# Kernel optimization log

Hardware: AMD Instinct MI355X
Metric: run time of the kernel (lower is better)

## Reference

```python
import jax, jax.numpy as jnp
import numpy as np
from jax import lax

ALPHA = 0.2  # LeakyReLU negative slope


def setup_inputs() -> dict:
    key = jax.random.key(0)
    k1, k2, k3, k4, k5 = jax.random.split(key, 5)
    B, Cin, N, L = 16, 64, 1024, 12
    Cout, Kt = 64, 3
    inp = jax.random.normal(k1, (B, Cin, N, L), dtype=jnp.float32)
    adj = jax.random.normal(k2, (B, N, N), dtype=jnp.float32)
    w0 = jax.random.normal(k3, (Cout, Cin, 1, Kt), dtype=jnp.float32) * (1.0 / np.sqrt(Cin * Kt))
    b0 = jax.random.normal(k4, (Cout,), dtype=jnp.float32) * 0.01
    w1 = jax.random.normal(k5, (1, Cout * L, 1), dtype=jnp.float32) * (1.0 / np.sqrt(Cout * L))
    return {"input": inp, "adj": adj, "w0": w0, "b0": b0, "w1": w1}


def reference(input, adj, w0, b0, w1):
    # conv0: Conv2d(in,out,(1,Kt),padding=(0,1)) -> (B, Cout, N, L)
    x = lax.conv_general_dilated(
        input, w0, window_strides=(1, 1), padding=((0, 0), (1, 1)),
        dimension_numbers=("NCHW", "OIHW", "NCHW"))
    x = x + b0[None, :, None, None]
    B, C, N, L = x.shape
    # permute(0,1,3,2).view(B, C*L, N): channel-major over (C, L)
    x1 = jnp.transpose(x, (0, 1, 3, 2)).reshape(B, C * L, N)
    # conv1 (k=1, no bias) applied twice (original uses conv1 for both f_1 and f_2)
    f = jnp.einsum('bkn,k->bn', x1, w1[0, :, 0])  # (B, N)
    # logits[b,i,j] = f_1[b,0,j] + f_2[b,i,0]
    logits = f[:, None, :] + f[:, :, None]  # (B, N, N)
    z = jnp.where(logits >= 0, logits, ALPHA * logits) + adj
    attention = jax.nn.softmax(z, axis=-1)
    attention = jnp.swapaxes(attention, -1, -2)  # (B, N, N)
    h_prime = jnp.einsum('bcnl,bnq->bcql', x, attention)
    return h_prime, attention
```

## Files before the change

kernel.cpp:

```cpp
#include <hip/hip_runtime.h>
#include <stdint.h>

typedef unsigned short ushort_t;
typedef unsigned int uint_t;

#define B_SZ 16
#define CIN 64
#define COUT 64
#define N_SZ 1024
#define L_SZ 12
#define CL 768
#define ALPHA 0.2f

typedef __bf16 bf16x8 __attribute__((ext_vector_type(8)));
typedef float floatx4 __attribute__((ext_vector_type(4)));

__device__ __forceinline__ ushort_t f2bf(float x) {
    uint_t u = __float_as_uint(x);
    u += 0x7fffu + ((u >> 16) & 1u);
    return (ushort_t)(u >> 16);
}
__device__ __forceinline__ float bf2f(ushort_t h) {
    return __uint_as_float(((uint_t)h) << 16);
}

__global__ __launch_bounds__(256) void conv_f_kernel(
    const float* __restrict__ inp, const float* __restrict__ w0,
    const float* __restrict__ b0, const float* __restrict__ w1,
    ushort_t* __restrict__ Xt, float* __restrict__ fout)
{
    __shared__ float Din[4 * 64 * 15];
    __shared__ float w0L[64 * 16 * 3];
    __shared__ float w1L[16 * 12];
    __shared__ float fred[256];

    const int n0 = blockIdx.x * 64;
    const int cb = blockIdx.y * 16;
    const int b  = blockIdx.z;
    const int t  = threadIdx.x;
    const int n_l = t & 63, ct = t >> 6;

    for (int idx = t; idx < 3072; idx += 256) {
        const int co_l = idx / 192, rem = idx - co_l * 192;
        const int ci = rem / 3, kt = rem - ci * 3;
        w0L[ci * 48 + co_l * 3 + kt] = w0[cb * 192 + idx];
    }
    if (t < 192) w1L[t] = w1[cb * 12 + t];
    for (int q = t; q < 512; q += 256) {
        const int ci = q >> 7, r = q & 127;
        Din[ci * 960 + (r & 63) * 15 + ((r >> 6) ? 13 : 0)] = 0.f;
    }

    float acc[4][12];
#pragma unroll
    for (int c = 0; c < 4; c++)
#pragma unroll
        for (int l = 0; l < 12; l++) acc[c][l] = 0.f;

    const float* inpB = inp + (size_t)b * CIN * N_SZ * L_SZ + n0 * 12;

    for (int cc = 0; cc < 16; cc++) {
        __syncthreads();
#pragma unroll
        for (int it = 0; it < 3; it++) {
            const int idx = it * 256 + t;
            const int ci_c = idx / 192, r = idx - ci_c * 192;
            const int n = r / 3, lg = r - n * 3;
            const float4 v = *(const float4*)(
                inpB + (size_t)(cc * 4 + ci_c) * (N_SZ * L_SZ) + n * 12 + lg * 4);
            float* d = &Din[ci_c * 960 + n * 15 + 1 + lg * 4];
            d[0] = v.x; d[1] = v.y; d[2] = v.z; d[3] = v.w;
        }
        __syncthreads();
#pragma unroll
        for (int cl = 0; cl < 4; cl++) {
            const int ci = cc * 4 + cl;
            const float* row = &Din[cl * 960 + n_l * 15];
            float p[14];
#pragma unroll
            for (int s = 0; s < 14; s++) p[s] = row[s];
            const float* wr = &w0L[ci * 48 + ct * 12];
#pragma unroll
            for (int c = 0; c < 4; c++) {
                const float wa = wr[c * 3], wb = wr[c * 3 + 1], wc = wr[c * 3 + 2];
#pragma unroll
                for (int l = 0; l < 12; l++)
                    acc[c][l] = fmaf(p[l], wa,
                                fmaf(p[l + 1], wb,
                                fmaf(p[l + 2], wc, acc[c][l])));
            }
        }
    }

    const int n = n0 + n_l;
    ushort_t* XtB = Xt + (size_t)b * CL * N_SZ + n;
    float fp = 0.f;
#pragma unroll
    for (int c = 0; c < 4; c++) {
        const int co_l = ct * 4 + c;
        const float b0v = b0[cb + co_l];
#pragma unroll
        for (int l = 0; l < 12; l++) {
            const float x = acc[c][l] + b0v;
            fp += x * w1L[co_l * 12 + l];
            XtB[(size_t)((cb + co_l) * 12 + l) * N_SZ] = f2bf(x);
        }
    }
    fred[t] = fp;
    __syncthreads();
    if (t < 64) {
        const float s = fred[t] + fred[t + 64] + fred[t + 128] + fred[t + 192];
        atomicAdd(&fout[b * N_SZ + n0 + t], s);
    }
}

__global__ __launch_bounds__(256) void softmax_kernel(
    const float* __restrict__ adj, const float* __restrict__ f,
    ushort_t* __restrict__ Sb)
{
    __shared__ float smx[4], sms[4];
    const int i = blockIdx.x, b = blockIdx.y, t = threadIdx.x;
    const int lane = t & 63, wv = t >> 6;

    const float* frow = f + b * N_SZ;
    const float fi = frow[i];
    const float4 fj = *(const float4*)(frow + 4 * t);
    const float4 av = *(const float4*)(adj + ((size_t)b * N_SZ + i) * N_SZ + 4 * t);

    float z[4];
    z[0] = fi + fj.x; z[1] = fi + fj.y; z[2] = fi + fj.z; z[3] = fi + fj.w;
#pragma unroll
    for (int k = 0; k < 4; k++) z[k] = (z[k] >= 0.f) ? z[k] : ALPHA * z[k];
    z[0] += av.x; z[1] += av.y; z[2] += av.z; z[3] += av.w;

    float mx = fmaxf(fmaxf(z[0], z[1]), fmaxf(z[2], z[3]));
#pragma unroll
    for (int o = 32; o; o >>= 1) mx = fmaxf(mx, __shfl_xor(mx, o, 64));
    if (lane == 0) smx[wv] = mx;
    __syncthreads();
    mx = fmaxf(fmaxf(smx[0], smx[1]), fmaxf(smx[2], smx[3]));

    float e[4], s = 0.f;
#pragma unroll
    for (int k = 0; k < 4; k++) { e[k] = __expf(z[k] - mx); s += e[k]; }
#pragma unroll
    for (int o = 32; o; o >>= 1) s += __shfl_xor(s, o, 64);
    if (lane == 0) sms[wv] = s;
    __syncthreads();
    s = sms[0] + sms[1] + sms[2] + sms[3];
    const float inv = 1.0f / s;

    const uint_t p0 = (uint_t)f2bf(e[0] * inv) | ((uint_t)f2bf(e[1] * inv) << 16);
    const uint_t p1 = (uint_t)f2bf(e[2] * inv) | ((uint_t)f2bf(e[3] * inv) << 16);
    uint2 pk; pk.x = p0; pk.y = p1;
    *(uint2*)&Sb[((size_t)b * N_SZ + i) * N_SZ + 4 * t] = pk;
}

__global__ __launch_bounds__(256) void att_transpose_kernel(
    const ushort_t* __restrict__ Sb, float* __restrict__ att)
{
    __shared__ float T[64][65];
    const int b = blockIdx.z;
    const int i0 = blockIdx.x * 64, j0 = blockIdx.y * 64;
    const int t = threadIdx.x;

#pragma unroll
    for (int ph = 0; ph < 2; ph++) {
        const int idx = ph * 256 + t;
        const int r = idx >> 3, c8 = (idx & 7) * 8;
        const uint4 v = *(const uint4*)(Sb + ((size_t)b * N_SZ + i0 + r) * N_SZ + j0 + c8);
        T[r][c8 + 0] = bf2f((ushort_t)(v.x & 0xffff));
        T[r][c8 + 1] = bf2f((ushort_t)(v.x >> 16));
        T[r][c8 + 2] = bf2f((ushort_t)(v.y & 0xffff));
        T[r][c8 + 3] = bf2f((ushort_t)(v.y >> 16));
        T[r][c8 + 4] = bf2f((ushort_t)(v.z & 0xffff));
        T[r][c8 + 5] = bf2f((ushort_t)(v.z >> 16));
        T[r][c8 + 6] = bf2f((ushort_t)(v.w & 0xffff));
        T[r][c8 + 7] = bf2f((ushort_t)(v.w >> 16));
    }
    __syncthreads();
#pragma unroll
    for (int ph = 0; ph < 4; ph++) {
        const int idx = ph * 256 + t;
        const int jr = idx >> 4, i4 = (idx & 15) * 4;
        float4 o;
        o.x = T[i4 + 0][jr]; o.y = T[i4 + 1][jr];
        o.z = T[i4 + 2][jr]; o.w = T[i4 + 3][jr];
        *(float4*)(att + ((size_t)b * N_SZ + j0 + jr) * N_SZ + i0 + i4) = o;
    }
}

__global__ __launch_bounds__(256) void gemm2_kernel(
    const ushort_t* __restrict__ Sb, const ushort_t* __restrict__ Xt,
    float* __restrict__ out)
{
    __shared__ ushort_t As[512 * 8];
    __shared__ ushort_t Bs[512 * 8];
    const int b = blockIdx.z;
    const int m0 = blockIdx.x * 128, q0 = blockIdx.y * 128;
    const int t = threadIdx.x;
    const int lane = t & 63, wv = t >> 6;
    const int wq = wv >> 1, wm = wv & 1;
    const int kc = lane >> 4, rr = lane & 15;

    const ushort_t* Sbase = Sb + (size_t)b * N_SZ * N_SZ;
    const ushort_t* Xbase = Xt + (size_t)b * CL * N_SZ;

    floatx4 acc[4][4];
#pragma unroll
    for (int i = 0; i < 4; i++)
#pragma unroll
        for (int j = 0; j < 4; j++) acc[i][j] = (floatx4)0.f;

    for (int k0 = 0; k0 < N_SZ; k0 += 32) {
        __syncthreads();
#pragma unroll
        for (int c = 0; c < 2; c++) {
            const int u = c * 256 + t;
            const int r = u & 127, kcs = u >> 7;
            *(uint4*)&As[u * 8] =
                *(const uint4*)(Sbase + (size_t)(q0 + r) * N_SZ + k0 + kcs * 8);
            *(uint4*)&Bs[u * 8] =
                *(const uint4*)(Xbase + (size_t)(m0 + r) * N_SZ + k0 + kcs * 8);
        }
        __syncthreads();

        bf16x8 af[4], bf[4];
#pragma unroll
        for (int i = 0; i < 4; i++) {
            af[i] = *(const bf16x8*)&As[(kc * 128 + wq * 64 + i * 16 + rr) * 8];
            bf[i] = *(const bf16x8*)&Bs[(kc * 128 + wm * 64 + i * 16 + rr) * 8];
        }
#pragma unroll
        for (int i = 0; i < 4; i++)
#pragma unroll
            for (int j = 0; j < 4; j++)
                acc[i][j] = __builtin_amdgcn_mfma_f32_16x16x32_bf16(
                    af[i], bf[j], acc[i][j], 0, 0, 0);
    }

#pragma unroll
    for (int j = 0; j < 4; j++) {
        const int m = m0 + wm * 64 + j * 16 + rr;
        const int co = m / 12, l = m - co * 12;
        float* ob = out + (size_t)(b * COUT + co) * (N_SZ * L_SZ) + l;
#pragma unroll
        for (int i = 0; i < 4; i++) {
            const int q = q0 + wq * 64 + i * 16 + kc * 4;
#pragma unroll
            for (int r2 = 0; r2 < 4; r2++)
                ob[(size_t)(q + r2) * 12] = acc[i][j][r2];
        }
    }
}

extern "C" void kernel_launch(void* const* d_in, const int* in_sizes, int n_in,
                              void* d_out, int out_size, void* d_ws, size_t ws_size,
                              hipStream_t stream)
{
    const float* inp = (const float*)d_in[0];
    const float* adj = (const float*)d_in[1];
    const float* w0  = (const float*)d_in[2];
    const float* b0  = (const float*)d_in[3];
    const float* w1  = (const float*)d_in[4];

    float* hprime = (float*)d_out;
    float* att    = hprime + (size_t)B_SZ * COUT * N_SZ * L_SZ;

    char* ws = (char*)d_ws;
    ushort_t* Xt = (ushort_t*)ws;
    ushort_t* Sb = (ushort_t*)(ws + (size_t)25165824);
    float*    fw = (float*)(ws + (size_t)25165824 + 33554432);

    hipMemsetAsync(fw, 0, B_SZ * N_SZ * sizeof(float), stream);
    conv_f_kernel<<<dim3(N_SZ / 64, 4, B_SZ), 256, 0, stream>>>(inp, w0, b0, w1, Xt, fw);
    softmax_kernel<<<dim3(N_SZ, B_SZ), 256, 0, stream>>>(adj, fw, Sb);
    att_transpose_kernel<<<dim3(N_SZ / 64, N_SZ / 64, B_SZ), 256, 0, stream>>>(Sb, att);
    gemm2_kernel<<<dim3(CL / 128, N_SZ / 128, B_SZ), 256, 0, stream>>>(Sb, Xt, hprime);
}
```

Baseline: 349.8 us.

## Load conv inputs directly into registers and use async global-to-LDS loads in GEMM

The conv kernel no longer stages inputs through shared memory. Each thread reads its own 12-element row straight from global memory, prefetching the next input channel while computing the current one, and handles the padding edges explicitly; launch bounds now request 4 blocks per CU. The GEMM tile loads now use global_load_lds so data goes to LDS without passing through VGPRs. This removes LDS traffic and barriers in the conv and frees registers in the GEMM. The per-thread float4 reads in the conv are strided by 48 bytes, and the async LDS path depends on the compiler and the hardware honoring the LDS layout and the wait semantics.

```diff
diff --git a/kernel.cpp b/kernel.cpp
--- a/kernel.cpp
+++ b/kernel.cpp
@@ -24,12 +24,16 @@
     return __uint_as_float(((uint_t)h) << 16);
 }
 
-__global__ __launch_bounds__(256) void conv_f_kernel(
+#define ASYNC16(ldsp, gp)                                                \
+    __builtin_amdgcn_global_load_lds(                                    \
+        (const __attribute__((address_space(1))) void*)(gp),             \
+        (__attribute__((address_space(3))) void*)(ldsp), 16, 0, 0)
+
+__global__ __launch_bounds__(256, 4) void conv_f_kernel(
     const float* __restrict__ inp, const float* __restrict__ w0,
     const float* __restrict__ b0, const float* __restrict__ w1,
     ushort_t* __restrict__ Xt, float* __restrict__ fout)
 {
-    __shared__ float Din[4 * 64 * 15];
     __shared__ float w0L[64 * 16 * 3];
     __shared__ float w1L[16 * 12];
     __shared__ float fred[256];
@@ -46,10 +50,7 @@
         w0L[ci * 48 + co_l * 3 + kt] = w0[cb * 192 + idx];
     }
     if (t < 192) w1L[t] = w1[cb * 12 + t];
-    for (int q = t; q < 512; q += 256) {
-        const int ci = q >> 7, r = q & 127;
-        Din[ci * 960 + (r & 63) * 15 + ((r >> 6) ? 13 : 0)] = 0.f;
-    }
+    __syncthreads();
 
     float acc[4][12];
 #pragma unroll
@@ -57,38 +58,46 @@
 #pragma unroll
         for (int l = 0; l < 12; l++) acc[c][l] = 0.f;
 
-    const float* inpB = inp + (size_t)b * CIN * N_SZ * L_SZ + n0 * 12;
-
-    for (int cc = 0; cc < 16; cc++) {
-        __syncthreads();
-#pragma unroll
-        for (int it = 0; it < 3; it++) {
-            const int idx = it * 256 + t;
-            const int ci_c = idx / 192, r = idx - ci_c * 192;
-            const int n = r / 3, lg = r - n * 3;
-            const float4 v = *(const float4*)(
-                inpB + (size_t)(cc * 4 + ci_c) * (N_SZ * L_SZ) + n * 12 + lg * 4);
-            float* d = &Din[ci_c * 960 + n * 15 + 1 + lg * 4];
-            d[0] = v.x; d[1] = v.y; d[2] = v.z; d[3] = v.w;
-        }
-        __syncthreads();
-#pragma unroll
-        for (int cl = 0; cl < 4; cl++) {
-            const int ci = cc * 4 + cl;
-            const float* row = &Din[cl * 960 + n_l * 15];
-            float p[14];
-#pragma unroll
-            for (int s = 0; s < 14; s++) p[s] = row[s];
-            const float* wr = &w0L[ci * 48 + ct * 12];
-#pragma unroll
-            for (int c = 0; c < 4; c++) {
-                const float wa = wr[c * 3], wb = wr[c * 3 + 1], wc = wr[c * 3 + 2];
-#pragma unroll
-                for (int l = 0; l < 12; l++)
-                    acc[c][l] = fmaf(p[l], wa,
-                                fmaf(p[l + 1], wb,
-                                fmaf(p[l + 2], wc, acc[c][l])));
-            }
+    const float* ib = inp + (size_t)b * CIN * N_SZ * L_SZ + (size_t)(n0 + n_l) * 12;
+
+    float4 c0 = *(const float4*)(ib);
+    float4 c1 = *(const float4*)(ib + 4);
+    float4 c2 = *(const float4*)(ib + 8);
+
+#pragma unroll 4
+    for (int ci = 0; ci < 63; ci++) {
+        const float* nb = ib + (size_t)(ci + 1) * (N_SZ * L_SZ);
+        const float4 x0 = *(const float4*)(nb);
+        const float4 x1 = *(const float4*)(nb + 4);
+        const float4 x2 = *(const float4*)(nb + 8);
+        const float p[12] = {c0.x, c0.y, c0.z, c0.w, c1.x, c1.y, c1.z, c1.w,
+                             c2.x, c2.y, c2.z, c2.w};
+        const float* wr = &w0L[ci * 48 + ct * 12];
+#pragma unroll
+        for (int c = 0; c < 4; c++) {
+            const float wa = wr[c * 3], wb = wr[c * 3 + 1], wc = wr[c * 3 + 2];
+            acc[c][0] = fmaf(p[0], wb, fmaf(p[1], wc, acc[c][0]));
+#pragma unroll
+            for (int l = 1; l < 11; l++)
+                acc[c][l] = fmaf(p[l - 1], wa,
+                            fmaf(p[l], wb, fmaf(p[l + 1], wc, acc[c][l])));
+            acc[c][11] = fmaf(p[10], wa, fmaf(p[11], wb, acc[c][11]));
+        }
+        c0 = x0; c1 = x1; c2 = x2;
+    }
+    {
+        const float p[12] = {c0.x, c0.y, c0.z, c0.w, c1.x, c1.y, c1.z, c1.w,
+                             c2.x, c2.y, c2.z, c2.w};
+        const float* wr = &w0L[63 * 48 + ct * 12];
+#pragma unroll
+        for (int c = 0; c < 4; c++) {
+            const float wa = wr[c * 3], wb = wr[c * 3 + 1], wc = wr[c * 3 + 2];
+            acc[c][0] = fmaf(p[0], wb, fmaf(p[1], wc, acc[c][0]));
+#pragma unroll
+            for (int l = 1; l < 11; l++)
+                acc[c][l] = fmaf(p[l - 1], wa,
+                            fmaf(p[l], wb, fmaf(p[l + 1], wc, acc[c][l])));
+            acc[c][11] = fmaf(p[10], wa, fmaf(p[11], wb, acc[c][11]));
         }
     }
 
@@ -218,25 +227,23 @@
         for (int c = 0; c < 2; c++) {
             const int u = c * 256 + t;
             const int r = u & 127, kcs = u >> 7;
-            *(uint4*)&As[u * 8] =
-                *(const uint4*)(Sbase + (size_t)(q0 + r) * N_SZ + k0 + kcs * 8);
-            *(uint4*)&Bs[u * 8] =
-                *(const uint4*)(Xbase + (size_t)(m0 + r) * N_SZ + k0 + kcs * 8);
+            ASYNC16(&As[u * 8], Sbase + (size_t)(q0 + r) * N_SZ + k0 + kcs * 8);
+            ASYNC16(&Bs[u * 8], Xbase + (size_t)(m0 + r) * N_SZ + k0 + kcs * 8);
         }
         __syncthreads();
 
-        bf16x8 af[4], bf[4];
+        bf16x8 af[4], bfr[4];
 #pragma unroll
         for (int i = 0; i < 4; i++) {
-            af[i] = *(const bf16x8*)&As[(kc * 128 + wq * 64 + i * 16 + rr) * 8];
-            bf[i] = *(const bf16x8*)&Bs[(kc * 128 + wm * 64 + i * 16 + rr) * 8];
+            af[i]  = *(const bf16x8*)&As[(kc * 128 + wq * 64 + i * 16 + rr) * 8];
+            bfr[i] = *(const bf16x8*)&Bs[(kc * 128 + wm * 64 + i * 16 + rr) * 8];
         }
 #pragma unroll
         for (int i = 0; i < 4; i++)
 #pragma unroll
             for (int j = 0; j < 4; j++)
                 acc[i][j] = __builtin_amdgcn_mfma_f32_16x16x32_bf16(
-                    af[i], bf[j], acc[i][j], 0, 0, 0);
+                    af[i], bfr[j], acc[i][j], 0, 0, 0);
     }
 
 #pragma unroll
```

Result: faster. 338.4 us (-3.3%).
